# Performance work log

Hardware: AMD Instinct MI355X
Metric: run time of the kernel (lower is better)

Reference implementation:

```python
import jax, jax.numpy as jnp
import numpy as np

B, X, Y, Z, C = 1, 16, 16, 16, 768
NUM_HEADS = 12


def setup_inputs() -> dict:
    key = jax.random.key(0)
    k0, k1, k2 = jax.random.split(key, 3)
    x = jax.random.normal(k0, (B, X, Y, Z, C), dtype=jnp.float32)
    # Linear weights stored as [in, out] (torch stores [out, in]; math is x @ W_in_out + b)
    w_qkv = jax.random.normal(k1, (C, 3 * C), dtype=jnp.float32) * 0.02
    b_qkv = jnp.zeros((3 * C,), dtype=jnp.float32)
    w_proj = jax.random.normal(k2, (C, C), dtype=jnp.float32) * 0.02
    b_proj = jnp.zeros((C,), dtype=jnp.float32)
    return {"x": x, "w_qkv": w_qkv, "b_qkv": b_qkv, "w_proj": w_proj, "b_proj": b_proj}


def reference(x, w_qkv, b_qkv, w_proj, b_proj):
    b, xx, yy, zz, c = x.shape
    h = NUM_HEADS
    hd = c // h
    scale = hd ** (-0.5)
    n = xx * yy * zz  # flatten 3D grid into tokens

    qkv = x.reshape(b, n, c) @ w_qkv + b_qkv          # [B, N, 3C]
    qkv = qkv.reshape(b, n, 3, h, hd).transpose(2, 0, 3, 1, 4)  # [3, B, H, N, hd]
    q, k, v = qkv[0], qkv[1], qkv[2]

    attn = jnp.einsum('bhnd,bhmd->bhnm', q * scale, k)  # [B, H, N, N]
    attn = jax.nn.softmax(attn, axis=-1)
    out = jnp.einsum('bhnm,bhmd->bhnd', attn, v)        # [B, H, N, hd]
    out = out.transpose(0, 2, 1, 3).reshape(b, n, c)
    out = out @ w_proj + b_proj
    return out.reshape(b, xx, yy, zz, c)
```

## Files before the change

kernel.cpp:

```cpp
#include <hip/hip_runtime.h>
#include <cstddef>

#define N_TOK 4096
#define C_DIM 768
#define H_NUM 12
#define C3    2304

typedef unsigned short u16;
using short8  = __attribute__((ext_vector_type(8))) short;
using floatx4 = __attribute__((ext_vector_type(4))) float;
using u16x4   = __attribute__((ext_vector_type(4))) u16;
using uint2v  = __attribute__((ext_vector_type(2))) unsigned;

#define K2SCALE 0.18033688011112043f

__device__ __forceinline__ u16 f2bf(float f) {
  union { float f; unsigned u; } v; v.f = f;
  unsigned r = v.u + 0x7FFFu + ((v.u >> 16) & 1u);
  return (u16)(r >> 16);
}

__device__ __forceinline__ unsigned permpack(float a, float b) {
  union { float f; unsigned u; } x, y; x.f = a; y.f = b;
  return __builtin_amdgcn_perm(y.u, x.u, 0x07060302u);
}

__device__ __forceinline__ float aexp2(float x) {
  float r;
  asm("v_exp_f32 %0, %1" : "=v"(r) : "v"(x));
  return r;
}

__device__ __forceinline__ void gload_lds16(const void* g, void* l) {
  __builtin_amdgcn_global_load_lds(
      (const __attribute__((address_space(1))) unsigned int*)g,
      (__attribute__((address_space(3))) unsigned int*)l, 16, 0, 0);
}

__global__ void k_pre(const float* __restrict__ x, u16* __restrict__ xb,
                      const float* __restrict__ wq, u16* __restrict__ wqT,
                      const float* __restrict__ wp, u16* __restrict__ wpT) {
  __shared__ float tile[32][33];
  const int b = blockIdx.x;
  if (b < 3072) {
    int i = b * 256 + threadIdx.x;
    float4 f = ((const float4*)x)[i];
    u16x4 o;
    o[0] = f2bf(f.x); o[1] = f2bf(f.y); o[2] = f2bf(f.z); o[3] = f2bf(f.w);
    ((u16x4*)xb)[i] = o;
    return;
  }
  const float* in; u16* out; int Cc, bx, by;
  if (b < 4800) { int t = b - 3072; in = wq; out = wqT; Cc = 2304; bx = t % 72; by = t / 72; }
  else          { int t = b - 4800; in = wp; out = wpT; Cc = 768;  bx = t % 24; by = t / 24; }
  const int R = 768;
  const int tx = threadIdx.x & 31;
  const int ty = threadIdx.x >> 5;
  const int c0 = bx * 32, r0 = by * 32;
#pragma unroll
  for (int i = 0; i < 32; i += 8)
    tile[ty + i][tx] = in[(size_t)(r0 + ty + i) * Cc + c0 + tx];
  __syncthreads();
#pragma unroll
  for (int i = 0; i < 32; i += 8)
    out[(size_t)(c0 + ty + i) * R + r0 + tx] = f2bf(tile[tx][ty + i]);
}

template <int MODE>
__global__ __launch_bounds__(256)
void k_gemm_bt(const u16* __restrict__ A, const u16* __restrict__ B,
               const float* __restrict__ bias, void* __restrict__ outp,
               u16* __restrict__ vT, int K) {
  __shared__ u16 As[128 * 32];
  __shared__ u16 Bs[128 * 32];
  const int tid  = threadIdx.x;
  const int wave = tid >> 6, lane = tid & 63, quad = lane >> 4, l16 = lane & 15;
  const int wrow = wave >> 1, wcol = wave & 1;
  const int bm = blockIdx.y, bn = blockIdx.x;
  const int r3 = l16 & 3;

  floatx4 acc[4][4];
#pragma unroll
  for (int i = 0; i < 4; ++i)
#pragma unroll
    for (int j = 0; j < 4; ++j)
#pragma unroll
      for (int r = 0; r < 4; ++r) acc[i][j][r] = 0.f;

  const int ar = tid >> 2;
  const int ac = ((tid & 3) ^ (ar & 3)) * 8;
  const u16* gA = A + (size_t)(bm * 128 + ar) * K + ac;
  const u16* gB = B + (size_t)(bn * 128 + ar) * K + ac;
  u16* lA = &As[0] + tid * 8;
  u16* lB = &Bs[0] + tid * 8;

  for (int k0 = 0; k0 < K; k0 += 32) {
    gload_lds16(gA + k0,                  lA);
    gload_lds16(gA + k0 + (size_t)64 * K, lA + 2048);
    gload_lds16(gB + k0,                  lB);
    gload_lds16(gB + k0 + (size_t)64 * K, lB + 2048);
    __syncthreads();
    short8 af[4], bf[4];
#pragma unroll
    for (int t = 0; t < 4; ++t) {
      af[t] = *(const short8*)&As[(wrow * 64 + t * 16 + l16) * 32 + ((quad ^ r3) * 8)];
      bf[t] = *(const short8*)&Bs[(wcol * 64 + t * 16 + l16) * 32 + ((quad ^ r3) * 8)];
    }
#pragma unroll
    for (int tm = 0; tm < 4; ++tm)
#pragma unroll
      for (int tn = 0; tn < 4; ++tn)
        acc[tm][tn] = __builtin_amdgcn_mfma_f32_16x16x32_bf16(af[tm], bf[tn], acc[tm][tn], 0, 0, 0);
    __syncthreads();
  }

  if (MODE == 0) {
    u16* qkv = (u16*)outp;
    const float qs = (bn < 6) ? K2SCALE : 1.0f;
#pragma unroll
    for (int tn = 0; tn < 4; ++tn) {
      const int col = bn * 128 + wcol * 64 + tn * 16 + l16;
      const float bc = bias[col];
      if (col < 1536) {
#pragma unroll
        for (int tm = 0; tm < 4; ++tm) {
          const int rowb = bm * 128 + wrow * 64 + tm * 16 + quad * 4;
#pragma unroll
          for (int r = 0; r < 4; ++r)
            qkv[(size_t)(rowb + r) * C3 + col] = f2bf((acc[tm][tn][r] + bc) * qs);
        }
      } else {
        const int hd_ = col - 1536;
#pragma unroll
        for (int tm = 0; tm < 4; ++tm) {
          const int rowb = bm * 128 + wrow * 64 + tm * 16 + quad * 4;
          u16x4 pk;
#pragma unroll
          for (int r = 0; r < 4; ++r) pk[r] = f2bf(acc[tm][tn][r] + bc);
          *(u16x4*)&vT[(size_t)hd_ * N_TOK + rowb] = pk;
        }
      }
    }
  } else {
    float* out = (float*)outp;
#pragma unroll
    for (int tn = 0; tn < 4; ++tn) {
      const int col = bn * 128 + wcol * 64 + tn * 16 + l16;
      const float bc = bias[col];
#pragma unroll
      for (int tm = 0; tm < 4; ++tm) {
        const int rowb = bm * 128 + wrow * 64 + tm * 16 + quad * 4;
#pragma unroll
        for (int r = 0; r < 4; ++r)
          out[(size_t)(rowb + r) * C_DIM + col] = acc[tm][tn][r] + bc;
      }
    }
  }
}

__global__ __launch_bounds__(128)
void k_flash(const u16* __restrict__ qkv, const u16* __restrict__ vT,
             u16* __restrict__ ao) {
  __shared__ u16 Ks[2][64 * 64];
  __shared__ u16 Vs[2][64 * 64];
  __shared__ u16 Ps[2][32 * 64];
  const int tid  = threadIdx.x;
  const int wave = tid >> 6, lane = tid & 63, quad = lane >> 4, l16 = lane & 15;
  const int h = blockIdx.x >> 6, qt = blockIdx.x & 63;
  const int lr = tid >> 3;
  const int lc = ((tid & 7) ^ (lr & 7)) * 8;
  const int r7 = l16 & 7;

  short8 bq[2][2];
#pragma unroll
  for (int qs = 0; qs < 2; ++qs)
#pragma unroll
    for (int ks = 0; ks < 2; ++ks)
      bq[qs][ks] = *(const short8*)&qkv[(size_t)(qt * 64 + wave * 32 + qs * 16 + l16) * C3
                                        + h * 64 + ks * 32 + quad * 8];

  const u16* gk = qkv + (size_t)lr * C3 + C_DIM + h * 64 + lc;
  const u16* gv = vT + (size_t)(h * 64 + lr) * N_TOK + lc;

  auto stage = [&](int b, int m0) {
#pragma unroll
    for (int p = 0; p < 4; ++p) {
      gload_lds16(gk + (size_t)(m0 + p * 16) * C3,        &Ks[b][p * 1024 + tid * 8]);
      gload_lds16(gv + (size_t)(p * 16) * N_TOK + m0,     &Vs[b][p * 1024 + tid * 8]);
    }
  };

  floatx4 o0[4], o1[4], l0, l1, zv;
#pragma unroll
  for (int r = 0; r < 4; ++r) { zv[r] = 0.f; l0[r] = 0.f; l1[r] = 0.f; }
#pragma unroll
  for (int d = 0; d < 4; ++d)
#pragma unroll
    for (int r = 0; r < 4; ++r) { o0[d][r] = 0.f; o1[d][r] = 0.f; }

  short8 ones;
#pragma unroll
  for (int i = 0; i < 8; ++i) ones[i] = (short)0x3F80;

  u16* psw = &Ps[wave][0];

  auto compute = [&](int b) __attribute__((always_inline)) {
    const u16* kb = &Ks[b][0];
    const u16* vb = &Vs[b][0];
    floatx4 s0[4], s1[4];
#pragma unroll
    for (int tn = 0; tn < 4; ++tn) {
      short8 ak = *(const short8*)&kb[(tn * 16 + l16) * 64 + (quad ^ r7) * 8];
      s0[tn] = __builtin_amdgcn_mfma_f32_16x16x32_bf16(ak, bq[0][0], zv, 0, 0, 0);
      s1[tn] = __builtin_amdgcn_mfma_f32_16x16x32_bf16(ak, bq[1][0], zv, 0, 0, 0);
    }
#pragma unroll
    for (int tn = 0; tn < 4; ++tn) {
      short8 ak = *(const short8*)&kb[(tn * 16 + l16) * 64 + ((quad + 4) ^ r7) * 8];
      s0[tn] = __builtin_amdgcn_mfma_f32_16x16x32_bf16(ak, bq[0][1], s0[tn], 0, 0, 0);
      s1[tn] = __builtin_amdgcn_mfma_f32_16x16x32_bf16(ak, bq[1][1], s1[tn], 0, 0, 0);
    }
#pragma unroll
    for (int qs = 0; qs < 2; ++qs) {
      u16* pr = psw + qs * 1024;
#pragma unroll
      for (int tn = 0; tn < 4; ++tn) {
        floatx4 sv = qs ? s1[tn] : s0[tn];
        float p0 = aexp2(sv[0]);
        float p1 = aexp2(sv[1]);
        float p2 = aexp2(sv[2]);
        float p3 = aexp2(sv[3]);
        uint2v pk;
        pk[0] = permpack(p0, p1);
        pk[1] = permpack(p2, p3);
        *(uint2v*)&pr[l16 * 64 + ((2 * tn + (quad >> 1)) ^ r7) * 8 + (quad & 1) * 4] = pk;
      }
    }
#pragma unroll
    for (int ks = 0; ks < 2; ++ks) {
      short8 ap0 = *(const short8*)&psw[l16 * 64 + ((quad + 4 * ks) ^ r7) * 8];
      short8 ap1 = *(const short8*)&psw[(16 + l16) * 64 + ((quad + 4 * ks) ^ r7) * 8];
#pragma unroll
      for (int dt = 0; dt < 4; ++dt) {
        short8 bv = *(const short8*)&vb[(dt * 16 + l16) * 64 + ((quad + 4 * ks) ^ r7) * 8];
        o0[dt] = __builtin_amdgcn_mfma_f32_16x16x32_bf16(ap0, bv, o0[dt], 0, 0, 0);
        o1[dt] = __builtin_amdgcn_mfma_f32_16x16x32_bf16(ap1, bv, o1[dt], 0, 0, 0);
      }
      l0 = __builtin_amdgcn_mfma_f32_16x16x32_bf16(ap0, ones, l0, 0, 0, 0);
      l1 = __builtin_amdgcn_mfma_f32_16x16x32_bf16(ap1, ones, l1, 0, 0, 0);
    }
  };

  stage(0, 0);
  __syncthreads();
  int m0 = 64;
  for (int it2 = 0; it2 < 31; ++it2) {
    stage(1, m0); m0 += 64;
    compute(0);
    __syncthreads();
    stage(0, m0); m0 += 64;
    compute(1);
    __syncthreads();
  }
  stage(1, m0);
  compute(0);
  __syncthreads();
  compute(1);

#pragma unroll
  for (int r = 0; r < 4; ++r) {
    const float i0 = 1.0f / l0[r];
    const float i1 = 1.0f / l1[r];
    const int row0 = qt * 64 + wave * 32 + quad * 4 + r;
#pragma unroll
    for (int dt = 0; dt < 4; ++dt) {
      const int col = h * 64 + dt * 16 + l16;
      ao[(size_t)row0 * C_DIM + col]        = f2bf(o0[dt][r] * i0);
      ao[(size_t)(row0 + 16) * C_DIM + col] = f2bf(o1[dt][r] * i1);
    }
  }
}

extern "C" void kernel_launch(void* const* d_in, const int* in_sizes, int n_in,
                              void* d_out, int out_size, void* d_ws, size_t ws_size,
                              hipStream_t stream) {
  const float* x      = (const float*)d_in[0];
  const float* w_qkv  = (const float*)d_in[1];
  const float* b_qkv  = (const float*)d_in[2];
  const float* w_proj = (const float*)d_in[3];
  const float* b_proj = (const float*)d_in[4];
  float* out = (float*)d_out;

  u16* xb     = (u16*)d_ws;
  u16* wqkvT  = xb     + (size_t)N_TOK * C_DIM;
  u16* wprojT = wqkvT  + (size_t)C3 * C_DIM;
  u16* qkv    = wprojT + (size_t)C_DIM * C_DIM;
  u16* vT     = qkv    + (size_t)N_TOK * C3;
  u16* ao     = vT     + (size_t)C_DIM * N_TOK;

  k_pre<<<5376, 256, 0, stream>>>(x, xb, w_qkv, wqkvT, w_proj, wprojT);
  k_gemm_bt<0><<<dim3(C3 / 128, N_TOK / 128), 256, 0, stream>>>(xb, wqkvT, b_qkv, qkv, vT, C_DIM);
  k_flash<<<H_NUM * (N_TOK / 64), 128, 0, stream>>>(qkv, vT, ao);
  k_gemm_bt<1><<<dim3(C_DIM / 128, N_TOK / 128), 256, 0, stream>>>(ao, wprojT, b_proj, out, nullptr, C_DIM);
}
```

Measured before the change: 220.8 us.

## Split flash attention over two key halves with wider blocks and combine pass

After: 218.4 us. Within noise of the previous version (-1.0%).

```diff
diff --git a/kernel.cpp b/kernel.cpp
--- a/kernel.cpp
+++ b/kernel.cpp
@@ -28,6 +28,12 @@
 __device__ __forceinline__ float aexp2(float x) {
   float r;
   asm("v_exp_f32 %0, %1" : "=v"(r) : "v"(x));
+  return r;
+}
+
+__device__ __forceinline__ float arcp(float x) {
+  float r;
+  asm("v_rcp_f32 %0, %1" : "=v"(r) : "v"(x));
   return r;
 }
 
@@ -158,25 +164,26 @@
   }
 }
 
-__global__ __launch_bounds__(128)
+__global__ __launch_bounds__(256)
 void k_flash(const u16* __restrict__ qkv, const u16* __restrict__ vT,
-             u16* __restrict__ ao) {
+             float* __restrict__ Opart, float* __restrict__ lpart) {
   __shared__ u16 Ks[2][64 * 64];
   __shared__ u16 Vs[2][64 * 64];
-  __shared__ u16 Ps[2][32 * 64];
+  __shared__ u16 Ps[4][32 * 64];
   const int tid  = threadIdx.x;
   const int wave = tid >> 6, lane = tid & 63, quad = lane >> 4, l16 = lane & 15;
-  const int h = blockIdx.x >> 6, qt = blockIdx.x & 63;
+  const int qt = blockIdx.x, h = blockIdx.y, split = blockIdx.z;
   const int lr = tid >> 3;
   const int lc = ((tid & 7) ^ (lr & 7)) * 8;
   const int r7 = l16 & 7;
+  const int kb = split * 2048;
 
   short8 bq[2][2];
 #pragma unroll
   for (int qs = 0; qs < 2; ++qs)
 #pragma unroll
     for (int ks = 0; ks < 2; ++ks)
-      bq[qs][ks] = *(const short8*)&qkv[(size_t)(qt * 64 + wave * 32 + qs * 16 + l16) * C3
+      bq[qs][ks] = *(const short8*)&qkv[(size_t)(qt * 128 + wave * 32 + qs * 16 + l16) * C3
                                         + h * 64 + ks * 32 + quad * 8];
 
   const u16* gk = qkv + (size_t)lr * C3 + C_DIM + h * 64 + lc;
@@ -184,9 +191,9 @@
 
   auto stage = [&](int b, int m0) {
 #pragma unroll
-    for (int p = 0; p < 4; ++p) {
-      gload_lds16(gk + (size_t)(m0 + p * 16) * C3,        &Ks[b][p * 1024 + tid * 8]);
-      gload_lds16(gv + (size_t)(p * 16) * N_TOK + m0,     &Vs[b][p * 1024 + tid * 8]);
+    for (int p = 0; p < 2; ++p) {
+      gload_lds16(gk + (size_t)(m0 + p * 32) * C3,    &Ks[b][p * 2048 + tid * 8]);
+      gload_lds16(gv + (size_t)(p * 32) * N_TOK + m0, &Vs[b][p * 2048 + tid * 8]);
     }
   };
 
@@ -205,18 +212,18 @@
   u16* psw = &Ps[wave][0];
 
   auto compute = [&](int b) __attribute__((always_inline)) {
-    const u16* kb = &Ks[b][0];
-    const u16* vb = &Vs[b][0];
+    const u16* kbp = &Ks[b][0];
+    const u16* vb  = &Vs[b][0];
     floatx4 s0[4], s1[4];
 #pragma unroll
     for (int tn = 0; tn < 4; ++tn) {
-      short8 ak = *(const short8*)&kb[(tn * 16 + l16) * 64 + (quad ^ r7) * 8];
+      short8 ak = *(const short8*)&kbp[(tn * 16 + l16) * 64 + (quad ^ r7) * 8];
       s0[tn] = __builtin_amdgcn_mfma_f32_16x16x32_bf16(ak, bq[0][0], zv, 0, 0, 0);
       s1[tn] = __builtin_amdgcn_mfma_f32_16x16x32_bf16(ak, bq[1][0], zv, 0, 0, 0);
     }
 #pragma unroll
     for (int tn = 0; tn < 4; ++tn) {
-      short8 ak = *(const short8*)&kb[(tn * 16 + l16) * 64 + ((quad + 4) ^ r7) * 8];
+      short8 ak = *(const short8*)&kbp[(tn * 16 + l16) * 64 + ((quad + 4) ^ r7) * 8];
       s0[tn] = __builtin_amdgcn_mfma_f32_16x16x32_bf16(ak, bq[0][1], s0[tn], 0, 0, 0);
       s1[tn] = __builtin_amdgcn_mfma_f32_16x16x32_bf16(ak, bq[1][1], s1[tn], 0, 0, 0);
     }
@@ -251,10 +258,10 @@
     }
   };
 
-  stage(0, 0);
+  stage(0, kb);
   __syncthreads();
-  int m0 = 64;
-  for (int it2 = 0; it2 < 31; ++it2) {
+  int m0 = kb + 64;
+  for (int it2 = 0; it2 < 15; ++it2) {
     stage(1, m0); m0 += 64;
     compute(0);
     __syncthreads();
@@ -267,18 +274,33 @@
   __syncthreads();
   compute(1);
 
+  const int rowg = qt * 128 + wave * 32 + quad * 4;
+  float* Ob = Opart + ((size_t)(split * H_NUM + h) * N_TOK) * 64;
+  float* lb = lpart + (size_t)(split * H_NUM + h) * N_TOK;
 #pragma unroll
   for (int r = 0; r < 4; ++r) {
-    const float i0 = 1.0f / l0[r];
-    const float i1 = 1.0f / l1[r];
-    const int row0 = qt * 64 + wave * 32 + quad * 4 + r;
 #pragma unroll
     for (int dt = 0; dt < 4; ++dt) {
-      const int col = h * 64 + dt * 16 + l16;
-      ao[(size_t)row0 * C_DIM + col]        = f2bf(o0[dt][r] * i0);
-      ao[(size_t)(row0 + 16) * C_DIM + col] = f2bf(o1[dt][r] * i1);
-    }
-  }
+      const int col = dt * 16 + l16;
+      Ob[(size_t)(rowg + r) * 64 + col]      = o0[dt][r];
+      Ob[(size_t)(rowg + 16 + r) * 64 + col] = o1[dt][r];
+    }
+    if (l16 == 0) {
+      lb[rowg + r]      = l0[r];
+      lb[rowg + 16 + r] = l1[r];
+    }
+  }
+}
+
+__global__ void k_combine(const float* __restrict__ Op, const float* __restrict__ lp,
+                          u16* __restrict__ ao) {
+  const int idx = blockIdx.x * 256 + threadIdx.x;
+  const int col = idx & 63;
+  const int row = idx >> 6;
+  const float o = Op[(size_t)row * 64 + col] + Op[((size_t)row + 49152) * 64 + col];
+  const float l = lp[row] + lp[row + 49152];
+  const int h = row >> 12, q = row & 4095;
+  ao[(size_t)q * C_DIM + h * 64 + col] = f2bf(o * arcp(l));
 }
 
 extern "C" void kernel_launch(void* const* d_in, const int* in_sizes, int n_in,
@@ -297,9 +319,12 @@
   u16* qkv    = wprojT + (size_t)C_DIM * C_DIM;
   u16* vT     = qkv    + (size_t)N_TOK * C3;
   u16* ao     = vT     + (size_t)C_DIM * N_TOK;
+  float* Opart = (float*)(ao + (size_t)N_TOK * C_DIM);
+  float* lpart = Opart + (size_t)2 * H_NUM * N_TOK * 64;
 
   k_pre<<<5376, 256, 0, stream>>>(x, xb, w_qkv, wqkvT, w_proj, wprojT);
   k_gemm_bt<0><<<dim3(C3 / 128, N_TOK / 128), 256, 0, stream>>>(xb, wqkvT, b_qkv, qkv, vT, C_DIM);
-  k_flash<<<H_NUM * (N_TOK / 64), 128, 0, stream>>>(qkv, vT, ao);
+  k_flash<<<dim3(N_TOK / 128, H_NUM, 2), 256, 0, stream>>>(qkv, vT, Opart, lpart);
+  k_combine<<<H_NUM * N_TOK * 64 / 256, 256, 0, stream>>>(Opart, lpart, ao);
   k_gemm_bt<1><<<dim3(C_DIM / 128, N_TOK / 128), 256, 0, stream>>>(ao, wprojT, b_proj, out, nullptr, C_DIM);
 }
```
